# Performance work log

Hardware: AMD Instinct MI355X
Metric: run time of the kernel (lower is better)

Reference implementation:

```python
import jax, jax.numpy as jnp
import numpy as np

DIM = 256
NUM_HEADS = 8
HEAD_DIM = DIM // NUM_HEADS
WS = 8                      # window size
N = WS * WS                 # tokens per window
TOPK = int(0.8 * N)         # 51
SCALE = HEAD_DIM ** -0.5
B_ = 2048                   # batch * num_windows


def _relative_position_index():
    # Swin-style relative position index, computed statically with numpy.
    coords_h = np.arange(WS)
    coords_w = np.arange(WS)
    coords = np.stack(np.meshgrid(coords_h, coords_w, indexing='ij'))  # (2, WS, WS)
    coords_flat = coords.reshape(2, -1)                                # (2, N)
    rel = coords_flat[:, :, None] - coords_flat[:, None, :]            # (2, N, N)
    rel = rel.transpose(1, 2, 0).astype(np.int64)                      # (N, N, 2)
    rel[:, :, 0] += WS - 1
    rel[:, :, 1] += WS - 1
    rel[:, :, 0] *= 2 * WS - 1
    idx = np.clip(rel.sum(-1), -1000, 1000)                            # (N, N)
    return jnp.asarray(idx)

REL_POS_INDEX = _relative_position_index()


def setup_inputs() -> dict:
    key = jax.random.key(0)
    ks = jax.random.split(key, 7)
    x = jax.random.normal(ks[0], (B_, N, DIM), dtype=jnp.float32)
    var = jax.random.normal(ks[1], (B_, N, DIM), dtype=jnp.float32)
    # parameters
    qkv_w = jax.random.normal(ks[2], (3 * DIM, DIM), dtype=jnp.float32) * (DIM ** -0.5)
    qkv_b = jnp.zeros((3 * DIM,), dtype=jnp.float32)
    proj_w = jax.random.normal(ks[3], (DIM, DIM), dtype=jnp.float32) * (DIM ** -0.5)
    proj_b = jnp.zeros((DIM,), dtype=jnp.float32)
    rpb_table = jax.random.normal(ks[4], ((2 * WS - 1) ** 2, NUM_HEADS), dtype=jnp.float32) * 0.02
    return {"x": x, "var": var, "qkv_w": qkv_w, "qkv_b": qkv_b,
            "proj_w": proj_w, "proj_b": proj_b, "rpb_table": rpb_table}


def reference(x, var, qkv_w, qkv_b, proj_w, proj_b, rpb_table):
    Bw, Nt, C = x.shape
    # --- topk-derived modulation map ---
    var_self = jnp.einsum('bnc,bmc->bnm', var, var)          # (B_, N, N)
    _, top_idx = jax.lax.top_k(var_self, TOPK)               # (B_, N, TOPK)
    mask = jnp.zeros((Bw, Nt, Nt), dtype=bool)
    mask = mask.at[jnp.arange(Bw)[:, None, None],
                   jnp.arange(Nt)[None, :, None],
                   top_idx].set(True)
    modulation = jnp.where(mask, 1.0, 1.2)[:, None]          # (B_, 1, N, N)

    # --- qkv projection ---
    qkv = x @ qkv_w.T + qkv_b                                # (B_, N, 3C)
    qkv = qkv.reshape(Bw, Nt, 3, NUM_HEADS, HEAD_DIM)
    qkv = jnp.transpose(qkv, (2, 0, 3, 1, 4))                # (3, B_, H, N, hd)
    q, k, v = qkv[0], qkv[1], qkv[2]
    q = q * SCALE

    # --- modulated attention with relative position bias ---
    scores = jnp.einsum('bhnd,bhmd->bhnm', q, k) * modulation  # (B_, H, N, N)
    rpb = rpb_table[REL_POS_INDEX.reshape(-1)].reshape(Nt, Nt, NUM_HEADS)
    rpb = jnp.transpose(rpb, (2, 0, 1))                        # (H, N, N)
    scores = scores + rpb[None]
    attn = jax.nn.softmax(scores, axis=-1)

    out = jnp.einsum('bhnm,bhmd->bhnd', attn, v)               # (B_, H, N, hd)
    out = jnp.transpose(out, (0, 2, 1, 3)).reshape(Bw, Nt, C)
    out = out @ proj_w.T + proj_b
    return out
```

## Files before the change

### kernel.cpp

```cpp
#include <hip/hip_runtime.h>

#define NT 64
#define DIMC 256
#define NHEADS 8
#define NWIN 2048
#define TOPK_ 51
#define SCALE_ 0.17677669529663687f


typedef short bf16x8 __attribute__((ext_vector_type(8)));
typedef float f32x4 __attribute__((ext_vector_type(4)));

#define MFMA16 __builtin_amdgcn_mfma_f32_16x16x32_bf16

__device__ __forceinline__ unsigned short f2bf(float f) {
    unsigned u = __float_as_uint(f);
    u += 0x7fffu + ((u >> 16) & 1u);
    return (unsigned short)(u >> 16);
}
__device__ __forceinline__ float bf2f(unsigned short h) {
    return __uint_as_float(((unsigned)h) << 16);
}
__device__ __forceinline__ void cvt8(const float* v, bf16x8& h, bf16x8& lo) {
#pragma unroll
    for (int j = 0; j < 8; ++j) {
        unsigned short hh = f2bf(v[j]);
        h[j] = (short)hh;
        lo[j] = (short)f2bf(v[j] - bf2f(hh));
    }
}

__global__ __launch_bounds__(256) void k_prep(
    const float* __restrict__ qkv_w, const float* __restrict__ proj_w,
    unsigned short* __restrict__ wqhi, unsigned short* __restrict__ wqlo,
    unsigned short* __restrict__ wphi, unsigned short* __restrict__ wplo)
{
    int e = blockIdx.x * 256 + threadIdx.x;
    float v; unsigned short* hi; unsigned short* lo; int di;
    if (e < 196608) {
        int j = e & 7, l = (e >> 3) & 63, ks = (e >> 9) & 7, ct = e >> 12;
        int o = ct * 16 + (l & 15);
        int k = ks * 32 + 8 * (l >> 4) + j;
        v = qkv_w[o * 256 + k]; hi = wqhi; lo = wqlo; di = e;
    } else {
        int e2 = e - 196608;
        int j = e2 & 7, l = (e2 >> 3) & 63, ks = (e2 >> 9) & 7, ct = e2 >> 12;
        int o = ct * 16 + (l & 15);
        int k = ks * 32 + 8 * (l >> 4) + j;
        v = proj_w[o * 256 + k]; hi = wphi; lo = wplo; di = e2;
    }
    unsigned short h = f2bf(v);
    hi[di] = h;
    lo[di] = f2bf(v - bf2f(h));
}

__global__ __launch_bounds__(256) void k_modulation(
    const float* __restrict__ var, unsigned long long* __restrict__ masks)
{
    __shared__ float vs[64][257];
    __shared__ float ss[64][65];
    __shared__ unsigned short bits[64][4];
    const int b = blockIdx.x, t = threadIdx.x;

    const float* vp = var + (size_t)b * (NT * DIMC);
    #pragma unroll
    for (int i = 0; i < 16; ++i) {
        int idx = t + i * 256;
        float4 v = reinterpret_cast<const float4*>(vp)[idx];
        int n = idx >> 6, k = (idx & 63) << 2;
        vs[n][k + 0] = v.x; vs[n][k + 1] = v.y; vs[n][k + 2] = v.z; vs[n][k + 3] = v.w;
    }
    __syncthreads();

    {
        const int n0 = (t >> 4) << 2, m0 = (t & 15) << 2;
        float acc[4][4];
        #pragma unroll
        for (int i = 0; i < 4; ++i)
            #pragma unroll
            for (int j = 0; j < 4; ++j) acc[i][j] = 0.f;
        #pragma unroll 4
        for (int k = 0; k < 256; ++k) {
            float av[4], bv[4];
            #pragma unroll
            for (int i = 0; i < 4; ++i) av[i] = vs[n0 + i][k];
            #pragma unroll
            for (int j = 0; j < 4; ++j) bv[j] = vs[m0 + j][k];
            #pragma unroll
            for (int i = 0; i < 4; ++i)
                #pragma unroll
                for (int j = 0; j < 4; ++j) acc[i][j] += av[i] * bv[j];
        }
        #pragma unroll
        for (int i = 0; i < 4; ++i)
            #pragma unroll
            for (int j = 0; j < 4; ++j) ss[n0 + i][m0 + j] = acc[i][j];
    }
    __syncthreads();

    {
        const int n = t >> 2, q = t & 3, mb = q * 16;
        float sv[16];
        int cnt[16];
        #pragma unroll
        for (int j = 0; j < 16; ++j) { sv[j] = ss[n][mb + j]; cnt[j] = 0; }
        for (int p = 0; p < 64; ++p) {
            float vv = ss[n][p];
            #pragma unroll
            for (int j = 0; j < 16; ++j)
                cnt[j] += (vv > sv[j] || (vv == sv[j] && p < mb + j)) ? 1 : 0;
        }
        unsigned int w = 0;
        #pragma unroll
        for (int j = 0; j < 16; ++j) if (cnt[j] < TOPK_) w |= (1u << j);
        bits[n][q] = (unsigned short)w;
    }
    __syncthreads();
    if (t < 64) {
        unsigned long long w =
            (unsigned long long)bits[t][0]
          | ((unsigned long long)bits[t][1] << 16)
          | ((unsigned long long)bits[t][2] << 32)
          | ((unsigned long long)bits[t][3] << 48);
        masks[(size_t)b * 64 + t] = w;
    }
}

__global__ __launch_bounds__(512) void k_attn(
    const float* __restrict__ x,
    const float* __restrict__ qkv_b,
    const float* __restrict__ rpb_table,
    const unsigned short* __restrict__ wqhi,
    const unsigned short* __restrict__ wqlo,
    const unsigned long long* __restrict__ masks,
    float* __restrict__ aout)
{
    __shared__ alignas(16) char smem[63008];
    unsigned short* qhi  = (unsigned short*)(smem);
    unsigned short* qlo  = (unsigned short*)(smem + 9216);
    unsigned short* khi  = (unsigned short*)(smem + 18432);
    unsigned short* klo  = (unsigned short*)(smem + 27648);
    unsigned short* phi  = (unsigned short*)(smem);
    unsigned short* plo  = (unsigned short*)(smem + 18432);
    unsigned short* vThi = (unsigned short*)(smem + 36864);
    unsigned short* vTlo = (unsigned short*)(smem + 46080);
    float* rpb_l = (float*)(smem + 55296);
    unsigned long long* mask_l = (unsigned long long*)(smem + 62496);

    const int b = blockIdx.x, t = threadIdx.x;
    const int l = t & 63, l15 = l & 15, lg = l >> 4;
    const int w = __builtin_amdgcn_readfirstlane(t >> 6);
    const int g_rt0 = 2 * (w & 1);
    const int g_pc0 = 3 * (w >> 1);
    const int hg = w >> 2;
    const int rs = w & 3;

    for (int i = t; i < 1800; i += 512) rpb_l[i] = rpb_table[i];
    if (t < 64) mask_l[t] = masks[(size_t)b * 64 + t];

    const float* xp = x + (size_t)b * (NT * DIMC);
    float* op = aout + (size_t)b * (NT * DIMC);

    for (int pass = 0; pass < 4; ++pass) {
        f32x4 acc[3][2];
        #pragma unroll
        for (int c = 0; c < 3; ++c) {
            const int pc = g_pc0 + c, mat = pc >> 2, within = pc & 3;
            const float bv = qkv_b[mat * 256 + (4 * pass + within) * 16 + l15];
            acc[c][0] = (f32x4){bv, bv, bv, bv};
            acc[c][1] = (f32x4){bv, bv, bv, bv};
        }
        for (int ks = 0; ks < 8; ++ks) {
            const float* a0p = xp + (g_rt0 * 16 + l15) * 256 + ks * 32 + lg * 8;
            const float* a1p = a0p + 16 * 256;
            float av0[8], av1[8];
            *reinterpret_cast<float4*>(&av0[0]) = *reinterpret_cast<const float4*>(a0p);
            *reinterpret_cast<float4*>(&av0[4]) = *reinterpret_cast<const float4*>(a0p + 4);
            *reinterpret_cast<float4*>(&av1[0]) = *reinterpret_cast<const float4*>(a1p);
            *reinterpret_cast<float4*>(&av1[4]) = *reinterpret_cast<const float4*>(a1p + 4);
            bf16x8 ah0, al0, ah1, al1;
            cvt8(av0, ah0, al0);
            cvt8(av1, ah1, al1);
            #pragma unroll
            for (int c = 0; c < 3; ++c) {
                const int pc = g_pc0 + c, mat = pc >> 2, within = pc & 3;
                const int ct = mat * 16 + 4 * pass + within;
                const bf16x8 bh = *reinterpret_cast<const bf16x8*>(wqhi + ct * 4096 + ks * 512 + l * 8);
                const bf16x8 bl = *reinterpret_cast<const bf16x8*>(wqlo + ct * 4096 + ks * 512 + l * 8);
                acc[c][0] = MFMA16(ah0, bh, acc[c][0], 0, 0, 0);
                acc[c][0] = MFMA16(ah0, bl, acc[c][0], 0, 0, 0);
                acc[c][0] = MFMA16(al0, bh, acc[c][0], 0, 0, 0);
                acc[c][1] = MFMA16(ah1, bh, acc[c][1], 0, 0, 0);
                acc[c][1] = MFMA16(ah1, bl, acc[c][1], 0, 0, 0);
                acc[c][1] = MFMA16(al1, bh, acc[c][1], 0, 0, 0);
            }
        }
        #pragma unroll
        for (int c = 0; c < 3; ++c) {
            const int pc = g_pc0 + c, mat = pc >> 2, within = pc & 3;
            const int hh = within >> 1, dh = within & 1;
            #pragma unroll
            for (int rtl = 0; rtl < 2; ++rtl) {
                const int tok0 = (g_rt0 + rtl) * 16 + 4 * lg;
                #pragma unroll
                for (int r = 0; r < 4; ++r) {
                    float val = acc[c][rtl][r];
                    const int tok = tok0 + r;
                    if (mat == 0) {
                        val *= SCALE_;
                        const unsigned short hv = f2bf(val);
                        qhi[tok * 72 + hh * 32 + dh * 16 + l15] = hv;
                        qlo[tok * 72 + hh * 32 + dh * 16 + l15] = f2bf(val - bf2f(hv));
                    } else if (mat == 1) {
                        const unsigned short hv = f2bf(val);
                        khi[tok * 72 + hh * 32 + dh * 16 + l15] = hv;
                        klo[tok * 72 + hh * 32 + dh * 16 + l15] = f2bf(val - bf2f(hv));
                    } else {
                        const int d = dh * 16 + l15;
                        const unsigned short hv = f2bf(val);
                        vThi[hh * 2304 + d * 72 + tok] = hv;
                        vTlo[hh * 2304 + d * 72 + tok] = f2bf(val - bf2f(hv));
                    }
                }
            }
        }
        __syncthreads();

        const int h = 2 * pass + hg;
        const bf16x8 aqh = *reinterpret_cast<const bf16x8*>(&qhi[(rs * 16 + l15) * 72 + hg * 32 + lg * 8]);
        const bf16x8 aql = *reinterpret_cast<const bf16x8*>(&qlo[(rs * 16 + l15) * 72 + hg * 32 + lg * 8]);
        f32x4 s[4];
        #pragma unroll
        for (int cs = 0; cs < 4; ++cs) {
            const bf16x8 bkh = *reinterpret_cast<const bf16x8*>(&khi[(cs * 16 + l15) * 72 + hg * 32 + lg * 8]);
            const bf16x8 bkl = *reinterpret_cast<const bf16x8*>(&klo[(cs * 16 + l15) * 72 + hg * 32 + lg * 8]);
            f32x4 z = (f32x4){0.f, 0.f, 0.f, 0.f};
            z = MFMA16(aqh, bkh, z, 0, 0, 0);
            z = MFMA16(aqh, bkl, z, 0, 0, 0);
            z = MFMA16(aql, bkh, z, 0, 0, 0);
            s[cs] = z;
        }
        const int srow0 = rs * 16 + 4 * lg;
        unsigned long long mw[4];
        #pragma unroll
        for (int r = 0; r < 4; ++r) mw[r] = mask_l[srow0 + r];
        float pbuf[4][4], mx[4], sm[4], inv[4];
        #pragma unroll
        for (int r = 0; r < 4; ++r) mx[r] = -1e30f;
        #pragma unroll
        for (int cs = 0; cs < 4; ++cs) {
            const int scol = cs * 16 + l15;
            #pragma unroll
            for (int r = 0; r < 4; ++r) {
                const int srow = srow0 + r;
                float sv = s[cs][r];
                sv *= ((mw[r] >> scol) & 1ull) ? 1.0f : 1.2f;
                const int ridx = ((srow >> 3) - (scol >> 3) + 7) * 15 + ((srow & 7) - (scol & 7) + 7);
                sv += rpb_l[ridx * NHEADS + h];
                pbuf[r][cs] = sv;
                mx[r] = fmaxf(mx[r], sv);
            }
        }
        #pragma unroll
        for (int r = 0; r < 4; ++r) {
            mx[r] = fmaxf(mx[r], __shfl_xor(mx[r], 1));
            mx[r] = fmaxf(mx[r], __shfl_xor(mx[r], 2));
            mx[r] = fmaxf(mx[r], __shfl_xor(mx[r], 4));
            mx[r] = fmaxf(mx[r], __shfl_xor(mx[r], 8));
            sm[r] = 0.f;
        }
        #pragma unroll
        for (int cs = 0; cs < 4; ++cs)
            #pragma unroll
            for (int r = 0; r < 4; ++r) {
                pbuf[r][cs] = __expf(pbuf[r][cs] - mx[r]);
                sm[r] += pbuf[r][cs];
            }
        #pragma unroll
        for (int r = 0; r < 4; ++r) {
            sm[r] += __shfl_xor(sm[r], 1);
            sm[r] += __shfl_xor(sm[r], 2);
            sm[r] += __shfl_xor(sm[r], 4);
            sm[r] += __shfl_xor(sm[r], 8);
            inv[r] = 1.f / sm[r];
        }
        __syncthreads();

        #pragma unroll
        for (int cs = 0; cs < 4; ++cs) {
            const int scol = cs * 16 + l15;
            #pragma unroll
            for (int r = 0; r < 4; ++r) {
                const float pp = pbuf[r][cs] * inv[r];
                const unsigned short ph = f2bf(pp);
                phi[hg * 4608 + (srow0 + r) * 72 + scol] = ph;
                plo[hg * 4608 + (srow0 + r) * 72 + scol] = f2bf(pp - bf2f(ph));
            }
        }
        __syncthreads();

        #pragma unroll
        for (int dt = 0; dt < 2; ++dt) {
            f32x4 o_ = (f32x4){0.f, 0.f, 0.f, 0.f};
            #pragma unroll
            for (int k2 = 0; k2 < 2; ++k2) {
                const bf16x8 pah = *reinterpret_cast<const bf16x8*>(&phi[hg * 4608 + (rs * 16 + l15) * 72 + k2 * 32 + lg * 8]);
                const bf16x8 pal = *reinterpret_cast<const bf16x8*>(&plo[hg * 4608 + (rs * 16 + l15) * 72 + k2 * 32 + lg * 8]);
                const bf16x8 vbh = *reinterpret_cast<const bf16x8*>(&vThi[hg * 2304 + (dt * 16 + l15) * 72 + k2 * 32 + lg * 8]);
                const bf16x8 vbl = *reinterpret_cast<const bf16x8*>(&vTlo[hg * 2304 + (dt * 16 + l15) * 72 + k2 * 32 + lg * 8]);
                o_ = MFMA16(pah, vbh, o_, 0, 0, 0);
                o_ = MFMA16(pah, vbl, o_, 0, 0, 0);
                o_ = MFMA16(pal, vbh, o_, 0, 0, 0);
            }
            #pragma unroll
            for (int r = 0; r < 4; ++r)
                op[(srow0 + r) * 256 + h * 32 + dt * 16 + l15] = o_[r];
        }
        __syncthreads();
    }
}

__global__ __launch_bounds__(512) void k_proj(
    const float* __restrict__ proj_b,
    const unsigned short* __restrict__ wphi,
    const unsigned short* __restrict__ wplo,
    float* __restrict__ inout)
{
    __shared__ alignas(16) unsigned short ahi[64][264];
    __shared__ alignas(16) unsigned short alo[64][264];
    const int b = blockIdx.x, t = threadIdx.x;
    const int l = t & 63;
    const int wave = __builtin_amdgcn_readfirstlane(t >> 6);

    float* base = inout + (size_t)b * (NT * DIMC);
    #pragma unroll
    for (int i = 0; i < 8; ++i) {
        int idx = t + i * 512;
        float4 v = reinterpret_cast<const float4*>(base)[idx];
        int n = idx >> 6, kq = (idx & 63) << 2;
        ushort4 h, lo;
        h.x = f2bf(v.x); h.y = f2bf(v.y); h.z = f2bf(v.z); h.w = f2bf(v.w);
        lo.x = f2bf(v.x - bf2f(h.x)); lo.y = f2bf(v.y - bf2f(h.y));
        lo.z = f2bf(v.z - bf2f(h.z)); lo.w = f2bf(v.w - bf2f(h.w));
        *reinterpret_cast<ushort4*>(&ahi[n][kq]) = h;
        *reinterpret_cast<ushort4*>(&alo[n][kq]) = lo;
    }
    __syncthreads();

    const int kgrp = 8 * (l >> 4);
    f32x4 acc[2][4];
    #pragma unroll
    for (int c = 0; c < 2; ++c) {
        const int col = (2 * wave + c) * 16 + (l & 15);
        const float bv = proj_b[col];
        #pragma unroll
        for (int r = 0; r < 4; ++r) acc[c][r] = (f32x4){bv, bv, bv, bv};
    }
    for (int ks = 0; ks < 8; ++ks) {
        bf16x8 ah0 = *reinterpret_cast<const bf16x8*>(&ahi[ 0 + (l & 15)][ks * 32 + kgrp]);
        bf16x8 al0 = *reinterpret_cast<const bf16x8*>(&alo[ 0 + (l & 15)][ks * 32 + kgrp]);
        bf16x8 ah1 = *reinterpret_cast<const bf16x8*>(&ahi[16 + (l & 15)][ks * 32 + kgrp]);
        bf16x8 al1 = *reinterpret_cast<const bf16x8*>(&alo[16 + (l & 15)][ks * 32 + kgrp]);
        bf16x8 ah2 = *reinterpret_cast<const bf16x8*>(&ahi[32 + (l & 15)][ks * 32 + kgrp]);
        bf16x8 al2 = *reinterpret_cast<const bf16x8*>(&alo[32 + (l & 15)][ks * 32 + kgrp]);
        bf16x8 ah3 = *reinterpret_cast<const bf16x8*>(&ahi[48 + (l & 15)][ks * 32 + kgrp]);
        bf16x8 al3 = *reinterpret_cast<const bf16x8*>(&alo[48 + (l & 15)][ks * 32 + kgrp]);
        #pragma unroll
        for (int c = 0; c < 2; ++c) {
            const int ct = 2 * wave + c;
            const int off = ct * 4096 + ks * 512 + l * 8;
            const bf16x8 bh = *reinterpret_cast<const bf16x8*>(wphi + off);
            const bf16x8 bl = *reinterpret_cast<const bf16x8*>(wplo + off);
            acc[c][0] = MFMA16(ah0, bh, acc[c][0], 0, 0, 0);
            acc[c][0] = MFMA16(ah0, bl, acc[c][0], 0, 0, 0);
            acc[c][0] = MFMA16(al0, bh, acc[c][0], 0, 0, 0);
            acc[c][1] = MFMA16(ah1, bh, acc[c][1], 0, 0, 0);
            acc[c][1] = MFMA16(ah1, bl, acc[c][1], 0, 0, 0);
            acc[c][1] = MFMA16(al1, bh, acc[c][1], 0, 0, 0);
            acc[c][2] = MFMA16(ah2, bh, acc[c][2], 0, 0, 0);
            acc[c][2] = MFMA16(ah2, bl, acc[c][2], 0, 0, 0);
            acc[c][2] = MFMA16(al2, bh, acc[c][2], 0, 0, 0);
            acc[c][3] = MFMA16(ah3, bh, acc[c][3], 0, 0, 0);
            acc[c][3] = MFMA16(ah3, bl, acc[c][3], 0, 0, 0);
            acc[c][3] = MFMA16(al3, bh, acc[c][3], 0, 0, 0);
        }
    }
    {
        const int rowo = 4 * (l >> 4);
        #pragma unroll
        for (int c = 0; c < 2; ++c) {
            const int col = (2 * wave + c) * 16 + (l & 15);
            #pragma unroll
            for (int rt = 0; rt < 4; ++rt) {
                #pragma unroll
                for (int r = 0; r < 4; ++r)
                    base[(rt * 16 + rowo + r) * 256 + col] = acc[c][rt][r];
            }
        }
    }
}

extern "C" void kernel_launch(void* const* d_in, const int* in_sizes, int n_in,
                              void* d_out, int out_size, void* d_ws, size_t ws_size,
                              hipStream_t stream)
{
    const float* x      = (const float*)d_in[0];
    const float* var    = (const float*)d_in[1];
    const float* qkv_w  = (const float*)d_in[2];
    const float* qkv_b  = (const float*)d_in[3];
    const float* proj_w = (const float*)d_in[4];
    const float* proj_b = (const float*)d_in[5];
    const float* rpb    = (const float*)d_in[6];
    float* out = (float*)d_out;

    unsigned short* wqhi = (unsigned short*)d_ws;
    unsigned short* wqlo = wqhi + 196608;
    unsigned short* wphi = wqlo + 196608;
    unsigned short* wplo = wphi + 65536;
    unsigned long long* masks = (unsigned long long*)((char*)d_ws + 1048576);

    k_prep      <<<1024, 256, 0, stream>>>(qkv_w, proj_w, wqhi, wqlo, wphi, wplo);
    k_modulation<<<NWIN, 256, 0, stream>>>(var, masks);
    k_attn      <<<NWIN, 512, 0, stream>>>(x, qkv_b, rpb, wqhi, wqlo, masks, out);
    k_proj      <<<NWIN, 512, 0, stream>>>(proj_b, wphi, wplo, out);
}
```

Before: 1.228 ms.

## Fuse output projection into attention kernel and stage x split-bf16 in LDS

The separate projection kernel is removed. Each attention pass now writes its per-head output as hi/lo bf16 into shared memory and accumulates the projection with MFMA, so the intermediate result no longer goes to global memory and back. x is loaded once and converted to hi/lo bf16 in LDS instead of being re-read and re-converted per pass. The modulation kernel moves to 512 threads with smaller per-thread tiles. LDS use grows to about 149KB, which limits occupancy to one block per CU.

```diff
diff --git a/kernel.cpp b/kernel.cpp
--- a/kernel.cpp
+++ b/kernel.cpp
@@ -21,13 +21,10 @@
 __device__ __forceinline__ float bf2f(unsigned short h) {
     return __uint_as_float(((unsigned)h) << 16);
 }
-__device__ __forceinline__ void cvt8(const float* v, bf16x8& h, bf16x8& lo) {
-#pragma unroll
-    for (int j = 0; j < 8; ++j) {
-        unsigned short hh = f2bf(v[j]);
-        h[j] = (short)hh;
-        lo[j] = (short)f2bf(v[j] - bf2f(hh));
-    }
+__device__ __forceinline__ void cvt4(const float4& v, ushort4& h, ushort4& lo) {
+    h.x = f2bf(v.x); h.y = f2bf(v.y); h.z = f2bf(v.z); h.w = f2bf(v.w);
+    lo.x = f2bf(v.x - bf2f(h.x)); lo.y = f2bf(v.y - bf2f(h.y));
+    lo.z = f2bf(v.z - bf2f(h.z)); lo.w = f2bf(v.w - bf2f(h.w));
 }
 
 __global__ __launch_bounds__(256) void k_prep(
@@ -54,18 +51,18 @@
     lo[di] = f2bf(v - bf2f(h));
 }
 
-__global__ __launch_bounds__(256) void k_modulation(
+__global__ __launch_bounds__(512) void k_modulation(
     const float* __restrict__ var, unsigned long long* __restrict__ masks)
 {
     __shared__ float vs[64][257];
     __shared__ float ss[64][65];
-    __shared__ unsigned short bits[64][4];
+    __shared__ alignas(8) unsigned char bits[64][8];
     const int b = blockIdx.x, t = threadIdx.x;
 
     const float* vp = var + (size_t)b * (NT * DIMC);
     #pragma unroll
-    for (int i = 0; i < 16; ++i) {
-        int idx = t + i * 256;
+    for (int i = 0; i < 8; ++i) {
+        int idx = t + i * 512;
         float4 v = reinterpret_cast<const float4*>(vp)[idx];
         int n = idx >> 6, k = (idx & 63) << 2;
         vs[n][k + 0] = v.x; vs[n][k + 1] = v.y; vs[n][k + 2] = v.z; vs[n][k + 3] = v.w;
@@ -73,79 +70,77 @@
     __syncthreads();
 
     {
-        const int n0 = (t >> 4) << 2, m0 = (t & 15) << 2;
-        float acc[4][4];
-        #pragma unroll
-        for (int i = 0; i < 4; ++i)
+        const int r0 = (t >> 4) << 1, c0 = (t & 15) << 2;
+        float acc[2][4];
+        #pragma unroll
+        for (int i = 0; i < 2; ++i)
             #pragma unroll
             for (int j = 0; j < 4; ++j) acc[i][j] = 0.f;
         #pragma unroll 4
         for (int k = 0; k < 256; ++k) {
-            float av[4], bv[4];
-            #pragma unroll
-            for (int i = 0; i < 4; ++i) av[i] = vs[n0 + i][k];
-            #pragma unroll
-            for (int j = 0; j < 4; ++j) bv[j] = vs[m0 + j][k];
-            #pragma unroll
-            for (int i = 0; i < 4; ++i)
-                #pragma unroll
-                for (int j = 0; j < 4; ++j) acc[i][j] += av[i] * bv[j];
-        }
-        #pragma unroll
-        for (int i = 0; i < 4; ++i)
-            #pragma unroll
-            for (int j = 0; j < 4; ++j) ss[n0 + i][m0 + j] = acc[i][j];
+            const float a0 = vs[r0][k], a1 = vs[r0 + 1][k];
+            float bv[4];
+            #pragma unroll
+            for (int j = 0; j < 4; ++j) bv[j] = vs[c0 + j][k];
+            #pragma unroll
+            for (int j = 0; j < 4; ++j) { acc[0][j] += a0 * bv[j]; acc[1][j] += a1 * bv[j]; }
+        }
+        #pragma unroll
+        for (int i = 0; i < 2; ++i)
+            #pragma unroll
+            for (int j = 0; j < 4; ++j) ss[r0 + i][c0 + j] = acc[i][j];
     }
     __syncthreads();
 
     {
-        const int n = t >> 2, q = t & 3, mb = q * 16;
-        float sv[16];
-        int cnt[16];
-        #pragma unroll
-        for (int j = 0; j < 16; ++j) { sv[j] = ss[n][mb + j]; cnt[j] = 0; }
+        const int n = t >> 3, q = t & 7, mb = q * 8;
+        float sv[8];
+        int cnt[8];
+        #pragma unroll
+        for (int j = 0; j < 8; ++j) { sv[j] = ss[n][mb + j]; cnt[j] = 0; }
         for (int p = 0; p < 64; ++p) {
-            float vv = ss[n][p];
-            #pragma unroll
-            for (int j = 0; j < 16; ++j)
+            const float vv = ss[n][p];
+            #pragma unroll
+            for (int j = 0; j < 8; ++j)
                 cnt[j] += (vv > sv[j] || (vv == sv[j] && p < mb + j)) ? 1 : 0;
         }
-        unsigned int w = 0;
-        #pragma unroll
-        for (int j = 0; j < 16; ++j) if (cnt[j] < TOPK_) w |= (1u << j);
-        bits[n][q] = (unsigned short)w;
+        unsigned w = 0;
+        #pragma unroll
+        for (int j = 0; j < 8; ++j) if (cnt[j] < TOPK_) w |= (1u << j);
+        bits[n][q] = (unsigned char)w;
     }
     __syncthreads();
-    if (t < 64) {
-        unsigned long long w =
-            (unsigned long long)bits[t][0]
-          | ((unsigned long long)bits[t][1] << 16)
-          | ((unsigned long long)bits[t][2] << 32)
-          | ((unsigned long long)bits[t][3] << 48);
-        masks[(size_t)b * 64 + t] = w;
-    }
+    if (t < 64)
+        masks[(size_t)b * 64 + t] = *reinterpret_cast<const unsigned long long*>(&bits[t][0]);
 }
 
 __global__ __launch_bounds__(512) void k_attn(
     const float* __restrict__ x,
     const float* __restrict__ qkv_b,
+    const float* __restrict__ proj_b,
     const float* __restrict__ rpb_table,
     const unsigned short* __restrict__ wqhi,
     const unsigned short* __restrict__ wqlo,
+    const unsigned short* __restrict__ wphi,
+    const unsigned short* __restrict__ wplo,
     const unsigned long long* __restrict__ masks,
-    float* __restrict__ aout)
+    float* __restrict__ out)
 {
-    __shared__ alignas(16) char smem[63008];
-    unsigned short* qhi  = (unsigned short*)(smem);
-    unsigned short* qlo  = (unsigned short*)(smem + 9216);
-    unsigned short* khi  = (unsigned short*)(smem + 18432);
-    unsigned short* klo  = (unsigned short*)(smem + 27648);
-    unsigned short* phi  = (unsigned short*)(smem);
-    unsigned short* plo  = (unsigned short*)(smem + 18432);
-    unsigned short* vThi = (unsigned short*)(smem + 36864);
-    unsigned short* vTlo = (unsigned short*)(smem + 46080);
-    float* rpb_l = (float*)(smem + 55296);
-    unsigned long long* mask_l = (unsigned long long*)(smem + 62496);
+    __shared__ alignas(16) char smem[149024];
+    unsigned short* xhi  = (unsigned short*)(smem);
+    unsigned short* xlo  = (unsigned short*)(smem + 33792);
+    unsigned short* qhi  = (unsigned short*)(smem + 67584);
+    unsigned short* qlo  = (unsigned short*)(smem + 76800);
+    unsigned short* khi  = (unsigned short*)(smem + 86016);
+    unsigned short* klo  = (unsigned short*)(smem + 95232);
+    unsigned short* phi  = (unsigned short*)(smem + 67584);
+    unsigned short* plo  = (unsigned short*)(smem + 86016);
+    unsigned short* vThi = (unsigned short*)(smem + 104448);
+    unsigned short* vTlo = (unsigned short*)(smem + 113664);
+    unsigned short* ohi  = (unsigned short*)(smem + 122880);
+    unsigned short* olo  = (unsigned short*)(smem + 132096);
+    float* rpb_l = (float*)(smem + 141312);
+    unsigned long long* mask_l = (unsigned long long*)(smem + 148512);
 
     const int b = blockIdx.x, t = threadIdx.x;
     const int l = t & 63, l15 = l & 15, lg = l >> 4;
@@ -155,11 +150,28 @@
     const int hg = w >> 2;
     const int rs = w & 3;
 
+    const float* xp = x + (size_t)b * (NT * DIMC);
+    #pragma unroll
+    for (int i = 0; i < 8; ++i) {
+        int idx = t + i * 512;
+        float4 v = reinterpret_cast<const float4*>(xp)[idx];
+        int n = idx >> 6, kq = (idx & 63) << 2;
+        ushort4 h, lo;
+        cvt4(v, h, lo);
+        *reinterpret_cast<ushort4*>(&xhi[n * 264 + kq]) = h;
+        *reinterpret_cast<ushort4*>(&xlo[n * 264 + kq]) = lo;
+    }
     for (int i = t; i < 1800; i += 512) rpb_l[i] = rpb_table[i];
     if (t < 64) mask_l[t] = masks[(size_t)b * 64 + t];
 
-    const float* xp = x + (size_t)b * (NT * DIMC);
-    float* op = aout + (size_t)b * (NT * DIMC);
+    f32x4 accp[2][4];
+    #pragma unroll
+    for (int c = 0; c < 2; ++c) {
+        const float bv = proj_b[(2 * w + c) * 16 + l15];
+        #pragma unroll
+        for (int rt = 0; rt < 4; ++rt) accp[c][rt] = (f32x4){bv, bv, bv, bv};
+    }
+    __syncthreads();
 
     for (int pass = 0; pass < 4; ++pass) {
         f32x4 acc[3][2];
@@ -171,16 +183,12 @@
             acc[c][1] = (f32x4){bv, bv, bv, bv};
         }
         for (int ks = 0; ks < 8; ++ks) {
-            const float* a0p = xp + (g_rt0 * 16 + l15) * 256 + ks * 32 + lg * 8;
-            const float* a1p = a0p + 16 * 256;
-            float av0[8], av1[8];
-            *reinterpret_cast<float4*>(&av0[0]) = *reinterpret_cast<const float4*>(a0p);
-            *reinterpret_cast<float4*>(&av0[4]) = *reinterpret_cast<const float4*>(a0p + 4);
-            *reinterpret_cast<float4*>(&av1[0]) = *reinterpret_cast<const float4*>(a1p);
-            *reinterpret_cast<float4*>(&av1[4]) = *reinterpret_cast<const float4*>(a1p + 4);
-            bf16x8 ah0, al0, ah1, al1;
-            cvt8(av0, ah0, al0);
-            cvt8(av1, ah1, al1);
+            const int a0 = (g_rt0 * 16 + l15) * 264 + ks * 32 + lg * 8;
+            const int a1 = a0 + 16 * 264;
+            const bf16x8 ah0 = *reinterpret_cast<const bf16x8*>(&xhi[a0]);
+            const bf16x8 al0 = *reinterpret_cast<const bf16x8*>(&xlo[a0]);
+            const bf16x8 ah1 = *reinterpret_cast<const bf16x8*>(&xhi[a1]);
+            const bf16x8 al1 = *reinterpret_cast<const bf16x8*>(&xlo[a1]);
             #pragma unroll
             for (int c = 0; c < 3; ++c) {
                 const int pc = g_pc0 + c, mat = pc >> 2, within = pc & 3;
@@ -313,88 +321,53 @@
                 o_ = MFMA16(pal, vbh, o_, 0, 0, 0);
             }
             #pragma unroll
-            for (int r = 0; r < 4; ++r)
-                op[(srow0 + r) * 256 + h * 32 + dt * 16 + l15] = o_[r];
-        }
-        __syncthreads();
-    }
-}
-
-__global__ __launch_bounds__(512) void k_proj(
-    const float* __restrict__ proj_b,
-    const unsigned short* __restrict__ wphi,
-    const unsigned short* __restrict__ wplo,
-    float* __restrict__ inout)
-{
-    __shared__ alignas(16) unsigned short ahi[64][264];
-    __shared__ alignas(16) unsigned short alo[64][264];
-    const int b = blockIdx.x, t = threadIdx.x;
-    const int l = t & 63;
-    const int wave = __builtin_amdgcn_readfirstlane(t >> 6);
-
-    float* base = inout + (size_t)b * (NT * DIMC);
-    #pragma unroll
-    for (int i = 0; i < 8; ++i) {
-        int idx = t + i * 512;
-        float4 v = reinterpret_cast<const float4*>(base)[idx];
-        int n = idx >> 6, kq = (idx & 63) << 2;
-        ushort4 h, lo;
-        h.x = f2bf(v.x); h.y = f2bf(v.y); h.z = f2bf(v.z); h.w = f2bf(v.w);
-        lo.x = f2bf(v.x - bf2f(h.x)); lo.y = f2bf(v.y - bf2f(h.y));
-        lo.z = f2bf(v.z - bf2f(h.z)); lo.w = f2bf(v.w - bf2f(h.w));
-        *reinterpret_cast<ushort4*>(&ahi[n][kq]) = h;
-        *reinterpret_cast<ushort4*>(&alo[n][kq]) = lo;
-    }
-    __syncthreads();
-
-    const int kgrp = 8 * (l >> 4);
-    f32x4 acc[2][4];
-    #pragma unroll
-    for (int c = 0; c < 2; ++c) {
-        const int col = (2 * wave + c) * 16 + (l & 15);
-        const float bv = proj_b[col];
-        #pragma unroll
-        for (int r = 0; r < 4; ++r) acc[c][r] = (f32x4){bv, bv, bv, bv};
-    }
-    for (int ks = 0; ks < 8; ++ks) {
-        bf16x8 ah0 = *reinterpret_cast<const bf16x8*>(&ahi[ 0 + (l & 15)][ks * 32 + kgrp]);
-        bf16x8 al0 = *reinterpret_cast<const bf16x8*>(&alo[ 0 + (l & 15)][ks * 32 + kgrp]);
-        bf16x8 ah1 = *reinterpret_cast<const bf16x8*>(&ahi[16 + (l & 15)][ks * 32 + kgrp]);
-        bf16x8 al1 = *reinterpret_cast<const bf16x8*>(&alo[16 + (l & 15)][ks * 32 + kgrp]);
-        bf16x8 ah2 = *reinterpret_cast<const bf16x8*>(&ahi[32 + (l & 15)][ks * 32 + kgrp]);
-        bf16x8 al2 = *reinterpret_cast<const bf16x8*>(&alo[32 + (l & 15)][ks * 32 + kgrp]);
-        bf16x8 ah3 = *reinterpret_cast<const bf16x8*>(&ahi[48 + (l & 15)][ks * 32 + kgrp]);
-        bf16x8 al3 = *reinterpret_cast<const bf16x8*>(&alo[48 + (l & 15)][ks * 32 + kgrp]);
+            for (int r = 0; r < 4; ++r) {
+                const float ov = o_[r];
+                const unsigned short hv = f2bf(ov);
+                const int oo = (srow0 + r) * 72 + hg * 32 + dt * 16 + l15;
+                ohi[oo] = hv;
+                olo[oo] = f2bf(ov - bf2f(hv));
+            }
+        }
+        __syncthreads();
+
+        #pragma unroll
+        for (int kk = 0; kk < 2; ++kk) {
+            const int ks = 2 * pass + kk;
+            bf16x8 bh[2], bl[2];
+            #pragma unroll
+            for (int c = 0; c < 2; ++c) {
+                const int ct = 2 * w + c;
+                bh[c] = *reinterpret_cast<const bf16x8*>(wphi + ct * 4096 + ks * 512 + l * 8);
+                bl[c] = *reinterpret_cast<const bf16x8*>(wplo + ct * 4096 + ks * 512 + l * 8);
+            }
+            #pragma unroll
+            for (int rt = 0; rt < 4; ++rt) {
+                const int ao = (rt * 16 + l15) * 72 + kk * 32 + lg * 8;
+                const bf16x8 ah = *reinterpret_cast<const bf16x8*>(&ohi[ao]);
+                const bf16x8 al = *reinterpret_cast<const bf16x8*>(&olo[ao]);
+                #pragma unroll
+                for (int c = 0; c < 2; ++c) {
+                    accp[c][rt] = MFMA16(ah, bh[c], accp[c][rt], 0, 0, 0);
+                    accp[c][rt] = MFMA16(ah, bl[c], accp[c][rt], 0, 0, 0);
+                    accp[c][rt] = MFMA16(al, bh[c], accp[c][rt], 0, 0, 0);
+                }
+            }
+        }
+        __syncthreads();
+    }
+
+    float* base = out + (size_t)b * (NT * DIMC);
+    {
+        const int rowo = 4 * lg;
         #pragma unroll
         for (int c = 0; c < 2; ++c) {
-            const int ct = 2 * wave + c;
-            const int off = ct * 4096 + ks * 512 + l * 8;
-            const bf16x8 bh = *reinterpret_cast<const bf16x8*>(wphi + off);
-            const bf16x8 bl = *reinterpret_cast<const bf16x8*>(wplo + off);
-            acc[c][0] = MFMA16(ah0, bh, acc[c][0], 0, 0, 0);
-            acc[c][0] = MFMA16(ah0, bl, acc[c][0], 0, 0, 0);
-            acc[c][0] = MFMA16(al0, bh, acc[c][0], 0, 0, 0);
-            acc[c][1] = MFMA16(ah1, bh, acc[c][1], 0, 0, 0);
-            acc[c][1] = MFMA16(ah1, bl, acc[c][1], 0, 0, 0);
-            acc[c][1] = MFMA16(al1, bh, acc[c][1], 0, 0, 0);
-            acc[c][2] = MFMA16(ah2, bh, acc[c][2], 0, 0, 0);
-            acc[c][2] = MFMA16(ah2, bl, acc[c][2], 0, 0, 0);
-            acc[c][2] = MFMA16(al2, bh, acc[c][2], 0, 0, 0);
-            acc[c][3] = MFMA16(ah3, bh, acc[c][3], 0, 0, 0);
-            acc[c][3] = MFMA16(ah3, bl, acc[c][3], 0, 0, 0);
-            acc[c][3] = MFMA16(al3, bh, acc[c][3], 0, 0, 0);
-        }
-    }
-    {
-        const int rowo = 4 * (l >> 4);
-        #pragma unroll
-        for (int c = 0; c < 2; ++c) {
-            const int col = (2 * wave + c) * 16 + (l & 15);
+            const int col = (2 * w + c) * 16 + l15;
             #pragma unroll
             for (int rt = 0; rt < 4; ++rt) {
                 #pragma unroll
                 for (int r = 0; r < 4; ++r)
-                    base[(rt * 16 + rowo + r) * 256 + col] = acc[c][rt][r];
+                    base[(rt * 16 + rowo + r) * 256 + col] = accp[c][rt][r];
             }
         }
     }
@@ -420,7 +393,6 @@
     unsigned long long* masks = (unsigned long long*)((char*)d_ws + 1048576);
 
     k_prep      <<<1024, 256, 0, stream>>>(qkv_w, proj_w, wqhi, wqlo, wphi, wplo);
-    k_modulation<<<NWIN, 256, 0, stream>>>(var, masks);
-    k_attn      <<<NWIN, 512, 0, stream>>>(x, qkv_b, rpb, wqhi, wqlo, masks, out);
-    k_proj      <<<NWIN, 512, 0, stream>>>(proj_b, wphi, wplo, out);
-}
+    k_modulation<<<NWIN, 512, 0, stream>>>(var, masks);
+    k_attn      <<<NWIN, 512, 0, stream>>>(x, qkv_b, proj_b, rpb, wqhi, wqlo, wphi, wplo, masks, out);
+}
```

Measured after the change: 1.283 ms. 1.05x slower.

## Pre-split x into bf16 hi/lo planes and widen modulation kernel to 512 threads

Applied to the files above, without the earlier changes.

Adds a separate kernel that converts x into bf16 hi/lo planes in workspace, so k_attn loads ready bf16x8 operands instead of fp32 values it converts itself. k_attn reads x once per pass across four passes, so the conversion cost is paid once rather than repeatedly. k_modulation moves to 512 threads with smaller per-thread tiles for the Gram matrix and the top-k count. The bf16 path only runs if the workspace is large enough; otherwise it falls back to the old path. The split adds an extra read and write pass over x in global memory, and the bf16 planes (same total size as the fp32 x) are read in every pass.

```diff
diff --git a/kernel.cpp b/kernel.cpp
--- a/kernel.cpp
+++ b/kernel.cpp
@@ -7,6 +7,7 @@
 #define TOPK_ 51
 #define SCALE_ 0.17677669529663687f
 
+#define PRESPLIT_NEED 136314880ull
 
 typedef short bf16x8 __attribute__((ext_vector_type(8)));
 typedef float f32x4 __attribute__((ext_vector_type(4)));
@@ -20,6 +21,11 @@
 }
 __device__ __forceinline__ float bf2f(unsigned short h) {
     return __uint_as_float(((unsigned)h) << 16);
+}
+__device__ __forceinline__ void cvt4(const float4& v, ushort4& h, ushort4& lo) {
+    h.x = f2bf(v.x); h.y = f2bf(v.y); h.z = f2bf(v.z); h.w = f2bf(v.w);
+    lo.x = f2bf(v.x - bf2f(h.x)); lo.y = f2bf(v.y - bf2f(h.y));
+    lo.z = f2bf(v.z - bf2f(h.z)); lo.w = f2bf(v.w - bf2f(h.w));
 }
 __device__ __forceinline__ void cvt8(const float* v, bf16x8& h, bf16x8& lo) {
 #pragma unroll
@@ -54,18 +60,34 @@
     lo[di] = f2bf(v - bf2f(h));
 }
 
-__global__ __launch_bounds__(256) void k_modulation(
+__global__ __launch_bounds__(256) void k_xsplit(
+    const float* __restrict__ x,
+    unsigned short* __restrict__ xsh, unsigned short* __restrict__ xsl)
+{
+    const int t = threadIdx.x;
+    #pragma unroll
+    for (int i = 0; i < 8; ++i) {
+        const size_t idx = (size_t)blockIdx.x * 2048 + i * 256 + t;
+        float4 v = reinterpret_cast<const float4*>(x)[idx];
+        ushort4 h, lo;
+        cvt4(v, h, lo);
+        reinterpret_cast<ushort4*>(xsh)[idx] = h;
+        reinterpret_cast<ushort4*>(xsl)[idx] = lo;
+    }
+}
+
+__global__ __launch_bounds__(512) void k_modulation(
     const float* __restrict__ var, unsigned long long* __restrict__ masks)
 {
     __shared__ float vs[64][257];
     __shared__ float ss[64][65];
-    __shared__ unsigned short bits[64][4];
+    __shared__ alignas(8) unsigned char bits[64][8];
     const int b = blockIdx.x, t = threadIdx.x;
 
     const float* vp = var + (size_t)b * (NT * DIMC);
     #pragma unroll
-    for (int i = 0; i < 16; ++i) {
-        int idx = t + i * 256;
+    for (int i = 0; i < 8; ++i) {
+        int idx = t + i * 512;
         float4 v = reinterpret_cast<const float4*>(vp)[idx];
         int n = idx >> 6, k = (idx & 63) << 2;
         vs[n][k + 0] = v.x; vs[n][k + 1] = v.y; vs[n][k + 2] = v.z; vs[n][k + 3] = v.w;
@@ -73,61 +95,55 @@
     __syncthreads();
 
     {
-        const int n0 = (t >> 4) << 2, m0 = (t & 15) << 2;
-        float acc[4][4];
-        #pragma unroll
-        for (int i = 0; i < 4; ++i)
+        const int r0 = (t >> 4) << 1, c0 = (t & 15) << 2;
+        float acc[2][4];
+        #pragma unroll
+        for (int i = 0; i < 2; ++i)
             #pragma unroll
             for (int j = 0; j < 4; ++j) acc[i][j] = 0.f;
         #pragma unroll 4
         for (int k = 0; k < 256; ++k) {
-            float av[4], bv[4];
-            #pragma unroll
-            for (int i = 0; i < 4; ++i) av[i] = vs[n0 + i][k];
-            #pragma unroll
-            for (int j = 0; j < 4; ++j) bv[j] = vs[m0 + j][k];
-            #pragma unroll
-            for (int i = 0; i < 4; ++i)
-                #pragma unroll
-                for (int j = 0; j < 4; ++j) acc[i][j] += av[i] * bv[j];
-        }
-        #pragma unroll
-        for (int i = 0; i < 4; ++i)
-            #pragma unroll
-            for (int j = 0; j < 4; ++j) ss[n0 + i][m0 + j] = acc[i][j];
+            const float a0 = vs[r0][k], a1 = vs[r0 + 1][k];
+            float bv[4];
+            #pragma unroll
+            for (int j = 0; j < 4; ++j) bv[j] = vs[c0 + j][k];
+            #pragma unroll
+            for (int j = 0; j < 4; ++j) { acc[0][j] += a0 * bv[j]; acc[1][j] += a1 * bv[j]; }
+        }
+        #pragma unroll
+        for (int i = 0; i < 2; ++i)
+            #pragma unroll
+            for (int j = 0; j < 4; ++j) ss[r0 + i][c0 + j] = acc[i][j];
     }
     __syncthreads();
 
     {
-        const int n = t >> 2, q = t & 3, mb = q * 16;
-        float sv[16];
-        int cnt[16];
-        #pragma unroll
-        for (int j = 0; j < 16; ++j) { sv[j] = ss[n][mb + j]; cnt[j] = 0; }
+        const int n = t >> 3, q = t & 7, mb = q * 8;
+        float sv[8];
+        int cnt[8];
+        #pragma unroll
+        for (int j = 0; j < 8; ++j) { sv[j] = ss[n][mb + j]; cnt[j] = 0; }
         for (int p = 0; p < 64; ++p) {
-            float vv = ss[n][p];
-            #pragma unroll
-            for (int j = 0; j < 16; ++j)
+            const float vv = ss[n][p];
+            #pragma unroll
+            for (int j = 0; j < 8; ++j)
                 cnt[j] += (vv > sv[j] || (vv == sv[j] && p < mb + j)) ? 1 : 0;
         }
-        unsigned int w = 0;
-        #pragma unroll
-        for (int j = 0; j < 16; ++j) if (cnt[j] < TOPK_) w |= (1u << j);
-        bits[n][q] = (unsigned short)w;
+        unsigned w = 0;
+        #pragma unroll
+        for (int j = 0; j < 8; ++j) if (cnt[j] < TOPK_) w |= (1u << j);
+        bits[n][q] = (unsigned char)w;
     }
     __syncthreads();
-    if (t < 64) {
-        unsigned long long w =
-            (unsigned long long)bits[t][0]
-          | ((unsigned long long)bits[t][1] << 16)
-          | ((unsigned long long)bits[t][2] << 32)
-          | ((unsigned long long)bits[t][3] << 48);
-        masks[(size_t)b * 64 + t] = w;
-    }
-}
-
+    if (t < 64)
+        masks[(size_t)b * 64 + t] = *reinterpret_cast<const unsigned long long*>(&bits[t][0]);
+}
+
+template<int MODE>
 __global__ __launch_bounds__(512) void k_attn(
     const float* __restrict__ x,
+    const unsigned short* __restrict__ xsh,
+    const unsigned short* __restrict__ xsl,
     const float* __restrict__ qkv_b,
     const float* __restrict__ rpb_table,
     const unsigned short* __restrict__ wqhi,
@@ -157,8 +173,11 @@
 
     for (int i = t; i < 1800; i += 512) rpb_l[i] = rpb_table[i];
     if (t < 64) mask_l[t] = masks[(size_t)b * 64 + t];
+    __syncthreads();
 
     const float* xp = x + (size_t)b * (NT * DIMC);
+    const unsigned short* xh = xsh + (size_t)b * (NT * DIMC);
+    const unsigned short* xl_ = xsl + (size_t)b * (NT * DIMC);
     float* op = aout + (size_t)b * (NT * DIMC);
 
     for (int pass = 0; pass < 4; ++pass) {
@@ -171,16 +190,23 @@
             acc[c][1] = (f32x4){bv, bv, bv, bv};
         }
         for (int ks = 0; ks < 8; ++ks) {
-            const float* a0p = xp + (g_rt0 * 16 + l15) * 256 + ks * 32 + lg * 8;
-            const float* a1p = a0p + 16 * 256;
-            float av0[8], av1[8];
-            *reinterpret_cast<float4*>(&av0[0]) = *reinterpret_cast<const float4*>(a0p);
-            *reinterpret_cast<float4*>(&av0[4]) = *reinterpret_cast<const float4*>(a0p + 4);
-            *reinterpret_cast<float4*>(&av1[0]) = *reinterpret_cast<const float4*>(a1p);
-            *reinterpret_cast<float4*>(&av1[4]) = *reinterpret_cast<const float4*>(a1p + 4);
             bf16x8 ah0, al0, ah1, al1;
-            cvt8(av0, ah0, al0);
-            cvt8(av1, ah1, al1);
+            const int a0 = (g_rt0 * 16 + l15) * 256 + ks * 32 + lg * 8;
+            const int a1 = a0 + 16 * 256;
+            if (MODE == 0) {
+                float av0[8], av1[8];
+                *reinterpret_cast<float4*>(&av0[0]) = *reinterpret_cast<const float4*>(xp + a0);
+                *reinterpret_cast<float4*>(&av0[4]) = *reinterpret_cast<const float4*>(xp + a0 + 4);
+                *reinterpret_cast<float4*>(&av1[0]) = *reinterpret_cast<const float4*>(xp + a1);
+                *reinterpret_cast<float4*>(&av1[4]) = *reinterpret_cast<const float4*>(xp + a1 + 4);
+                cvt8(av0, ah0, al0);
+                cvt8(av1, ah1, al1);
+            } else {
+                ah0 = *reinterpret_cast<const bf16x8*>(xh + a0);
+                al0 = *reinterpret_cast<const bf16x8*>(xl_ + a0);
+                ah1 = *reinterpret_cast<const bf16x8*>(xh + a1);
+                al1 = *reinterpret_cast<const bf16x8*>(xl_ + a1);
+            }
             #pragma unroll
             for (int c = 0; c < 3; ++c) {
                 const int pc = g_pc0 + c, mat = pc >> 2, within = pc & 3;
@@ -339,9 +365,7 @@
         float4 v = reinterpret_cast<const float4*>(base)[idx];
         int n = idx >> 6, kq = (idx & 63) << 2;
         ushort4 h, lo;
-        h.x = f2bf(v.x); h.y = f2bf(v.y); h.z = f2bf(v.z); h.w = f2bf(v.w);
-        lo.x = f2bf(v.x - bf2f(h.x)); lo.y = f2bf(v.y - bf2f(h.y));
-        lo.z = f2bf(v.z - bf2f(h.z)); lo.w = f2bf(v.w - bf2f(h.w));
+        cvt4(v, h, lo);
         *reinterpret_cast<ushort4*>(&ahi[n][kq]) = h;
         *reinterpret_cast<ushort4*>(&alo[n][kq]) = lo;
     }
@@ -418,9 +442,18 @@
     unsigned short* wphi = wqlo + 196608;
     unsigned short* wplo = wphi + 65536;
     unsigned long long* masks = (unsigned long long*)((char*)d_ws + 1048576);
+    unsigned short* xsh = (unsigned short*)((char*)d_ws + 2097152);
+    unsigned short* xsl = xsh + 33554432;
+
+    const bool presplit = (ws_size >= PRESPLIT_NEED);
 
     k_prep      <<<1024, 256, 0, stream>>>(qkv_w, proj_w, wqhi, wqlo, wphi, wplo);
-    k_modulation<<<NWIN, 256, 0, stream>>>(var, masks);
-    k_attn      <<<NWIN, 512, 0, stream>>>(x, qkv_b, rpb, wqhi, wqlo, masks, out);
+    k_modulation<<<NWIN, 512, 0, stream>>>(var, masks);
+    if (presplit) {
+        k_xsplit <<<4096, 256, 0, stream>>>(x, xsh, xsl);
+        k_attn<1><<<NWIN, 512, 0, stream>>>(x, xsh, xsl, qkv_b, rpb, wqhi, wqlo, masks, out);
+    } else {
+        k_attn<0><<<NWIN, 512, 0, stream>>>(x, xsh, xsl, qkv_b, rpb, wqhi, wqlo, masks, out);
+    }
     k_proj      <<<NWIN, 512, 0, stream>>>(proj_b, wphi, wplo, out);
 }
```

Result: no change. 1.210 ms (-1.4%).
